# Optimization experiments

Hardware: AMD Instinct MI355X
Metric: run time of the kernel (lower is better)

## Reference

```python
import jax, jax.numpy as jnp
import numpy as np

N_NODES = 100000
N_EDGES = 1600000
N_MOVES = 200000
D = 256          # in_channels
H = 512          # hidden_dim

def setup_inputs() -> dict:
    key = jax.random.key(0)
    ks = jax.random.split(key, 6)
    node_embeddings = jax.random.normal(ks[0], (N_NODES, D), dtype=jnp.float32)
    edge_index = jax.random.randint(ks[1], (2, N_EDGES), 0, N_NODES, dtype=jnp.int64)
    move_edge_idxs = jax.random.randint(ks[2], (N_MOVES,), 0, N_EDGES, dtype=jnp.int64)
    # torch Linear weights: [out, in], scaled like kaiming-uniform-ish
    W1 = jax.random.normal(ks[3], (H, 2 * D), dtype=jnp.float32) * (1.0 / np.sqrt(2 * D))
    b1 = jnp.zeros((H,), dtype=jnp.float32)
    W2 = jax.random.normal(ks[4], (H // 2, H), dtype=jnp.float32) * (1.0 / np.sqrt(H))
    b2 = jnp.zeros((H // 2,), dtype=jnp.float32)
    W3 = jax.random.normal(ks[5], (1, H // 2), dtype=jnp.float32) * (1.0 / np.sqrt(H // 2))
    b3 = jnp.zeros((1,), dtype=jnp.float32)
    return {"node_embeddings": node_embeddings, "edge_index": edge_index,
            "move_edge_idxs": move_edge_idxs, "W1": W1, "b1": b1,
            "W2": W2, "b2": b2, "W3": W3, "b3": b3}

def reference(node_embeddings, edge_index, move_edge_idxs, W1, b1, W2, b2, W3, b3):
    # candidate_moves = edge_index[:, move_edge_idxs].T -> [n_moves, 2]
    src = edge_index[0, move_edge_idxs]          # [n_moves]
    tgt = edge_index[1, move_edge_idxs]          # [n_moves]
    emb_src = node_embeddings[src]               # [n_moves, D]
    emb_tgt = node_embeddings[tgt]               # [n_moves, D]
    x = jnp.concatenate([emb_src, emb_tgt], axis=-1)   # [n_moves, 2D]
    # 3-layer MLP (dropout is identity in eval mode)
    h = jax.nn.relu(x @ W1.T + b1)               # [n_moves, H]
    h = jax.nn.relu(h @ W2.T + b2)               # [n_moves, H//2]
    logits = (h @ W3.T + b3).squeeze(-1)         # [n_moves]
    return logits
```

## Files before the change

kernel.cpp:

```cpp
#include <hip/hip_runtime.h>
#include <hip/hip_bf16.h>

typedef __attribute__((ext_vector_type(4))) float f32x4;
typedef __attribute__((ext_vector_type(8))) short bfrag;
typedef __attribute__((ext_vector_type(4))) float facc;
typedef __attribute__((ext_vector_type(8))) ushort u16x8;

#define N_MOVES 200000
#define N_EDGES 1600000
#define DEMB 256
#define KD 512
#define H1D 512
#define H2D 256
#define MT 64
#define NTHREADS 512

__device__ __forceinline__ ushort f2b(float f) {
  union { float f; unsigned u; } x; x.f = f;
  unsigned r = (x.u + 0x7fffu + ((x.u >> 16) & 1u)) >> 16;
  return (ushort)r;
}
__device__ __forceinline__ float b2f(ushort h) {
  union { unsigned u; float f; } x; x.u = ((unsigned)h) << 16;
  return x.f;
}

__global__ void convert_w(const float* __restrict__ W1, const float* __restrict__ W2,
                          ushort* __restrict__ Wb) {
  int i = (blockIdx.x * 256 + threadIdx.x) * 4;
  const int n1 = H1D * KD;
  if (i < n1) {
    f32x4 v = *(const f32x4*)(W1 + i);
    ushort4 h = { f2b(v.x), f2b(v.y), f2b(v.z), f2b(v.w) };
    *(ushort4*)(Wb + i) = h;
  } else {
    int j = i - n1;
    f32x4 v = *(const f32x4*)(W2 + j);
    ushort4 h = { f2b(v.x), f2b(v.y), f2b(v.z), f2b(v.w) };
    *(ushort4*)(Wb + n1 + j) = h;
  }
}

__global__ void convert_emb(const float* __restrict__ E, ushort* __restrict__ Eb) {
  int i = (blockIdx.x * 256 + threadIdx.x) * 8;
  f32x4 a = *(const f32x4*)(E + i);
  f32x4 b = *(const f32x4*)(E + i + 4);
  u16x8 h = { f2b(a.x), f2b(a.y), f2b(a.z), f2b(a.w),
              f2b(b.x), f2b(b.y), f2b(b.z), f2b(b.w) };
  *(u16x8*)(Eb + i) = h;
}

template<int EMBBF>
__global__ __launch_bounds__(NTHREADS, 2)
void fused_mlp(const float* __restrict__ emb,
               const ushort* __restrict__ embb,
               const int* __restrict__ edge_index,
               const int* __restrict__ move_idx,
               const ushort* __restrict__ W1b,
               const float* __restrict__ b1,
               const ushort* __restrict__ W2b,
               const float* __restrict__ b2,
               const float* __restrict__ W3,
               const float* __restrict__ b3,
               float* __restrict__ out)
{
  __shared__ ushort bufA[MT][KD];
  __shared__ ushort bufB[MT][KD];
  __shared__ int   s_src[MT], s_tgt[MT];
  __shared__ float sW3[H2D];

  const int tid  = threadIdx.x;
  const int lane = tid & 63;
  const int wave = tid >> 6;
  const int m0   = blockIdx.x * MT;

  if (tid < MT) {
    int e = move_idx[m0 + tid];
    s_src[tid] = edge_index[e];
    s_tgt[tid] = edge_index[N_EDGES + e];
  }
  if (tid < H2D) sW3[tid] = W3[tid];
  __syncthreads();

  const int arow = lane & 15;
  const int akE  = (lane >> 4) << 3;
  const int akB  = (lane >> 4) << 4;
  const int nq   = (lane >> 4) << 2;

  const ushort* wp0 = W1b + (size_t)(((wave << 6) + arow) * KD) + akE;
  const ushort* wp1 = wp0 + 16 * KD;
  const ushort* wp2 = wp0 + 32 * KD;
  const ushort* wp3 = wp0 + 48 * KD;

  bfrag bA[4], bB[4];
  bA[0] = *(const bfrag*)(wp0);      bA[1] = *(const bfrag*)(wp1);
  bA[2] = *(const bfrag*)(wp2);      bA[3] = *(const bfrag*)(wp3);
  bB[0] = *(const bfrag*)(wp0 + 32); bB[1] = *(const bfrag*)(wp1 + 32);
  bB[2] = *(const bfrag*)(wp2 + 32); bB[3] = *(const bfrag*)(wp3 + 32);

  if (EMBBF) {
    #pragma unroll
    for (int it = 0; it < 8; ++it) {
      int row  = (wave << 3) + it;
      int gl   = lane ^ (row & 7);
      int node = (gl < 32) ? s_src[row] : s_tgt[row];
      const ushort* gp = embb + (size_t)node * DEMB + ((size_t)(gl & 31) << 3);
      __builtin_amdgcn_global_load_lds(
          (const __attribute__((address_space(1))) void*)gp,
          (__attribute__((address_space(3))) void*)(&bufA[row][0]),
          16, 0, 0);
    }
  } else {
    for (int u = tid; u < MT * 128; u += NTHREADS) {
      int row = u >> 7;
      int c4  = u & 127;
      const float* sp = (c4 < 64) ? (emb + (size_t)s_src[row] * DEMB + (c4 << 2))
                                  : (emb + (size_t)s_tgt[row] * DEMB + ((c4 - 64) << 2));
      f32x4 v = *(const f32x4*)sp;
      ushort4 h = { f2b(v.x), f2b(v.y), f2b(v.z), f2b(v.w) };
      int bo = (c4 << 3) ^ ((row & 7) << 4);
      *(ushort4*)((char*)(&bufA[row][0]) + bo) = h;
    }
  }
  __syncthreads();

  facc acc[4][4];
  #pragma unroll
  for (int ng = 0; ng < 4; ++ng) {
    f32x4 bv = *(const f32x4*)(b1 + (wave << 6) + (ng << 4) + nq);
    #pragma unroll
    for (int mg = 0; mg < 4; ++mg) acc[mg][ng] = bv;
  }

  bfrag aE[4], aO[4];
  #pragma unroll
  for (int mg = 0; mg < 4; ++mg) {
    int row = (mg << 4) + arow;
    int bo = akB ^ ((row & 7) << 4);
    aE[mg] = *(const bfrag*)((const char*)(&bufA[row][0]) + bo);
  }

  #pragma unroll
  for (int kk2 = 0; kk2 < 8; ++kk2) {
    const int kk = kk2 << 1;
    if (kk + 1 < 16) {
      #pragma unroll
      for (int mg = 0; mg < 4; ++mg) {
        int row = (mg << 4) + arow;
        int bo = (((kk + 1) << 6) + akB) ^ ((row & 7) << 4);
        aO[mg] = *(const bfrag*)((const char*)(&bufA[row][0]) + bo);
      }
    }
    __builtin_amdgcn_s_setprio(1);
    #pragma unroll
    for (int mg = 0; mg < 4; ++mg)
      #pragma unroll
      for (int ng = 0; ng < 4; ++ng)
        acc[mg][ng] = __builtin_amdgcn_mfma_f32_16x16x32_bf16(bA[ng], aE[mg], acc[mg][ng], 0, 0, 0);
    __builtin_amdgcn_s_setprio(0);
    if (kk + 2 < 16) {
      bA[0] = *(const bfrag*)(wp0 + ((kk + 2) << 5));
      bA[1] = *(const bfrag*)(wp1 + ((kk + 2) << 5));
      bA[2] = *(const bfrag*)(wp2 + ((kk + 2) << 5));
      bA[3] = *(const bfrag*)(wp3 + ((kk + 2) << 5));
      #pragma unroll
      for (int mg = 0; mg < 4; ++mg) {
        int row = (mg << 4) + arow;
        int bo = (((kk + 2) << 6) + akB) ^ ((row & 7) << 4);
        aE[mg] = *(const bfrag*)((const char*)(&bufA[row][0]) + bo);
      }
    }
    __builtin_amdgcn_s_setprio(1);
    #pragma unroll
    for (int mg = 0; mg < 4; ++mg)
      #pragma unroll
      for (int ng = 0; ng < 4; ++ng)
        acc[mg][ng] = __builtin_amdgcn_mfma_f32_16x16x32_bf16(bB[ng], aO[mg], acc[mg][ng], 0, 0, 0);
    __builtin_amdgcn_s_setprio(0);
    if (kk + 3 < 16) {
      bB[0] = *(const bfrag*)(wp0 + ((kk + 3) << 5));
      bB[1] = *(const bfrag*)(wp1 + ((kk + 3) << 5));
      bB[2] = *(const bfrag*)(wp2 + ((kk + 3) << 5));
      bB[3] = *(const bfrag*)(wp3 + ((kk + 3) << 5));
    }
  }

  const ushort* cp0 = W2b + (size_t)(((wave << 5) + arow) * KD) + akE;
  const ushort* cp1 = cp0 + 16 * KD;
  bfrag cA[2], cB[2];
  cA[0] = *(const bfrag*)(cp0);      cA[1] = *(const bfrag*)(cp1);
  cB[0] = *(const bfrag*)(cp0 + 32); cB[1] = *(const bfrag*)(cp1 + 32);

  #pragma unroll
  for (int mg = 0; mg < 4; ++mg) {
    int m = (mg << 4) + arow;
    #pragma unroll
    for (int ng = 0; ng < 4; ++ng) {
      int nb = (wave << 6) + (ng << 4) + nq;
      ushort4 h;
      h.x = f2b(fmaxf(acc[mg][ng][0], 0.f));
      h.y = f2b(fmaxf(acc[mg][ng][1], 0.f));
      h.z = f2b(fmaxf(acc[mg][ng][2], 0.f));
      h.w = f2b(fmaxf(acc[mg][ng][3], 0.f));
      int bo = (nb << 1) ^ ((m & 7) << 4);
      *(ushort4*)((char*)(&bufB[0][0]) + m * (KD * 2) + bo) = h;
    }
  }
  __syncthreads();

  facc acc2[4][2];
  #pragma unroll
  for (int ng = 0; ng < 2; ++ng) {
    f32x4 bv = *(const f32x4*)(b2 + (wave << 5) + (ng << 4) + nq);
    #pragma unroll
    for (int mg = 0; mg < 4; ++mg) acc2[mg][ng] = bv;
  }

  #pragma unroll
  for (int mg = 0; mg < 4; ++mg) {
    int row = (mg << 4) + arow;
    int bo = akB ^ ((row & 7) << 4);
    aE[mg] = *(const bfrag*)((const char*)(&bufB[row][0]) + bo);
  }

  #pragma unroll
  for (int kk2 = 0; kk2 < 8; ++kk2) {
    const int kk = kk2 << 1;
    if (kk + 1 < 16) {
      #pragma unroll
      for (int mg = 0; mg < 4; ++mg) {
        int row = (mg << 4) + arow;
        int bo = (((kk + 1) << 6) + akB) ^ ((row & 7) << 4);
        aO[mg] = *(const bfrag*)((const char*)(&bufB[row][0]) + bo);
      }
    }
    __builtin_amdgcn_s_setprio(1);
    #pragma unroll
    for (int mg = 0; mg < 4; ++mg)
      #pragma unroll
      for (int ng = 0; ng < 2; ++ng)
        acc2[mg][ng] = __builtin_amdgcn_mfma_f32_16x16x32_bf16(cA[ng], aE[mg], acc2[mg][ng], 0, 0, 0);
    __builtin_amdgcn_s_setprio(0);
    if (kk + 2 < 16) {
      cA[0] = *(const bfrag*)(cp0 + ((kk + 2) << 5));
      cA[1] = *(const bfrag*)(cp1 + ((kk + 2) << 5));
      #pragma unroll
      for (int mg = 0; mg < 4; ++mg) {
        int row = (mg << 4) + arow;
        int bo = (((kk + 2) << 6) + akB) ^ ((row & 7) << 4);
        aE[mg] = *(const bfrag*)((const char*)(&bufB[row][0]) + bo);
      }
    }
    __builtin_amdgcn_s_setprio(1);
    #pragma unroll
    for (int mg = 0; mg < 4; ++mg)
      #pragma unroll
      for (int ng = 0; ng < 2; ++ng)
        acc2[mg][ng] = __builtin_amdgcn_mfma_f32_16x16x32_bf16(cB[ng], aO[mg], acc2[mg][ng], 0, 0, 0);
    __builtin_amdgcn_s_setprio(0);
    if (kk + 3 < 16) {
      cB[0] = *(const bfrag*)(cp0 + ((kk + 3) << 5));
      cB[1] = *(const bfrag*)(cp1 + ((kk + 3) << 5));
    }
  }

  ushort (*H2s)[H2D] = (ushort(*)[H2D])bufA;
  #pragma unroll
  for (int mg = 0; mg < 4; ++mg) {
    int m = (mg << 4) + arow;
    #pragma unroll
    for (int ng = 0; ng < 2; ++ng) {
      int nb = (wave << 5) + (ng << 4) + nq;
      ushort4 h;
      h.x = f2b(fmaxf(acc2[mg][ng][0], 0.f));
      h.y = f2b(fmaxf(acc2[mg][ng][1], 0.f));
      h.z = f2b(fmaxf(acc2[mg][ng][2], 0.f));
      h.w = f2b(fmaxf(acc2[mg][ng][3], 0.f));
      int bo = (nb << 1) ^ ((m & 7) << 4);
      *(ushort4*)((char*)(&H2s[0][0]) + m * (H2D * 2) + bo) = h;
    }
  }
  __syncthreads();

  {
    const float b3v = b3[0];
    int row = tid >> 3;
    int oct = tid & 7;
    float sum = 0.f;
    #pragma unroll
    for (int j = 0; j < 4; ++j) {
      int kb = (oct << 6) + (j << 4);
      int bo = kb ^ ((row & 7) << 4);
      bfrag hv = *(const bfrag*)((const char*)(&H2s[row][0]) + bo);
      int k0 = (oct << 5) + (j << 3);
      #pragma unroll
      for (int e = 0; e < 8; ++e)
        sum += b2f((ushort)hv[e]) * sW3[k0 + e];
    }
    sum += __shfl_xor(sum, 1);
    sum += __shfl_xor(sum, 2);
    sum += __shfl_xor(sum, 4);
    if (oct == 0) out[m0 + row] = sum + b3v;
  }
}

extern "C" void kernel_launch(void* const* d_in, const int* in_sizes, int n_in,
                              void* d_out, int out_size, void* d_ws, size_t ws_size,
                              hipStream_t stream) {
  const float* emb        = (const float*)d_in[0];
  const int*   edge_index = (const int*)d_in[1];
  const int*   move_idx   = (const int*)d_in[2];
  const float* W1         = (const float*)d_in[3];
  const float* b1         = (const float*)d_in[4];
  const float* W2         = (const float*)d_in[5];
  const float* b2         = (const float*)d_in[6];
  const float* W3         = (const float*)d_in[7];
  const float* b3         = (const float*)d_in[8];
  float* out = (float*)d_out;

  ushort* Wb   = (ushort*)d_ws;
  ushort* Embb = Wb + (H1D * KD + H2D * KD);
  const size_t need = (size_t)(H1D * KD + H2D * KD + 100000 * DEMB) * 2;

  convert_w<<<384, 256, 0, stream>>>(W1, W2, Wb);

  if (ws_size >= need) {
    convert_emb<<<12500, 256, 0, stream>>>(emb, Embb);
    fused_mlp<1><<<N_MOVES / MT, NTHREADS, 0, stream>>>(
        emb, Embb, edge_index, move_idx,
        Wb, b1, Wb + H1D * KD, b2, W3, b3, out);
  } else {
    fused_mlp<0><<<N_MOVES / MT, NTHREADS, 0, stream>>>(
        emb, Embb, edge_index, move_idx,
        Wb, b1, Wb + H1D * KD, b2, W3, b3, out);
  }
}
```

Baseline: 524.7 us.

## Double move tile to 128 rows and reuse one LDS buffer for hidden activations

The fused MLP block now handles 128 moves with 1024 threads. Each wave owns a narrower slice of output columns across more rows, so each weight fragment read from global memory is reused over twice as many rows. The separate layer-2 input buffer is dropped, and layer-1 outputs are written back into the gather buffer after an extra barrier, which keeps LDS at one 128KB buffer per block. In exchange, each LDS A-fragment now feeds fewer MFMAs, so there is more LDS traffic per MFMA. A CU likely holds only one large block, so barriers stall all of its waves together. Bounds checks for a partial last tile are added.

```diff
diff --git a/kernel.cpp b/kernel.cpp
--- a/kernel.cpp
+++ b/kernel.cpp
@@ -12,8 +12,8 @@
 #define KD 512
 #define H1D 512
 #define H2D 256
-#define MT 64
-#define NTHREADS 512
+#define MT 128
+#define NTHREADS 1024
 
 __device__ __forceinline__ ushort f2b(float f) {
   union { float f; unsigned u; } x; x.f = f;
@@ -51,7 +51,7 @@
 }
 
 template<int EMBBF>
-__global__ __launch_bounds__(NTHREADS, 2)
+__global__ __launch_bounds__(NTHREADS, 4)
 void fused_mlp(const float* __restrict__ emb,
                const ushort* __restrict__ embb,
                const int* __restrict__ edge_index,
@@ -65,7 +65,6 @@
                float* __restrict__ out)
 {
   __shared__ ushort bufA[MT][KD];
-  __shared__ ushort bufB[MT][KD];
   __shared__ int   s_src[MT], s_tgt[MT];
   __shared__ float sW3[H2D];
 
@@ -75,7 +74,9 @@
   const int m0   = blockIdx.x * MT;
 
   if (tid < MT) {
-    int e = move_idx[m0 + tid];
+    int mi = m0 + tid;
+    if (mi >= N_MOVES) mi = N_MOVES - 1;
+    int e = move_idx[mi];
     s_src[tid] = edge_index[e];
     s_tgt[tid] = edge_index[N_EDGES + e];
   }
@@ -87,16 +88,15 @@
   const int akB  = (lane >> 4) << 4;
   const int nq   = (lane >> 4) << 2;
 
-  const ushort* wp0 = W1b + (size_t)(((wave << 6) + arow) * KD) + akE;
+  const ushort* wp0 = W1b + (size_t)(((wave << 5) + arow) * KD) + akE;
   const ushort* wp1 = wp0 + 16 * KD;
-  const ushort* wp2 = wp0 + 32 * KD;
-  const ushort* wp3 = wp0 + 48 * KD;
-
-  bfrag bA[4], bB[4];
+
+  bfrag bA[2], bB[2];
   bA[0] = *(const bfrag*)(wp0);      bA[1] = *(const bfrag*)(wp1);
-  bA[2] = *(const bfrag*)(wp2);      bA[3] = *(const bfrag*)(wp3);
   bB[0] = *(const bfrag*)(wp0 + 32); bB[1] = *(const bfrag*)(wp1 + 32);
-  bB[2] = *(const bfrag*)(wp2 + 32); bB[3] = *(const bfrag*)(wp3 + 32);
+  f32x4 bv1[2];
+  bv1[0] = *(const f32x4*)(b1 + (wave << 5) + nq);
+  bv1[1] = *(const f32x4*)(b1 + (wave << 5) + 16 + nq);
 
   if (EMBBF) {
     #pragma unroll
@@ -124,17 +124,13 @@
   }
   __syncthreads();
 
-  facc acc[4][4];
-  #pragma unroll
-  for (int ng = 0; ng < 4; ++ng) {
-    f32x4 bv = *(const f32x4*)(b1 + (wave << 6) + (ng << 4) + nq);
-    #pragma unroll
-    for (int mg = 0; mg < 4; ++mg) acc[mg][ng] = bv;
-  }
-
-  bfrag aE[4], aO[4];
-  #pragma unroll
-  for (int mg = 0; mg < 4; ++mg) {
+  facc acc[8][2];
+  #pragma unroll
+  for (int mg = 0; mg < 8; ++mg) { acc[mg][0] = bv1[0]; acc[mg][1] = bv1[1]; }
+
+  bfrag aE[8];
+  #pragma unroll
+  for (int mg = 0; mg < 8; ++mg) {
     int row = (mg << 4) + arow;
     int bo = akB ^ ((row & 7) << 4);
     aE[mg] = *(const bfrag*)((const char*)(&bufA[row][0]) + bo);
@@ -143,142 +139,123 @@
   #pragma unroll
   for (int kk2 = 0; kk2 < 8; ++kk2) {
     const int kk = kk2 << 1;
-    if (kk + 1 < 16) {
-      #pragma unroll
-      for (int mg = 0; mg < 4; ++mg) {
-        int row = (mg << 4) + arow;
-        int bo = (((kk + 1) << 6) + akB) ^ ((row & 7) << 4);
-        aO[mg] = *(const bfrag*)((const char*)(&bufA[row][0]) + bo);
-      }
-    }
     __builtin_amdgcn_s_setprio(1);
     #pragma unroll
-    for (int mg = 0; mg < 4; ++mg)
-      #pragma unroll
-      for (int ng = 0; ng < 4; ++ng)
-        acc[mg][ng] = __builtin_amdgcn_mfma_f32_16x16x32_bf16(bA[ng], aE[mg], acc[mg][ng], 0, 0, 0);
+    for (int mg = 0; mg < 8; ++mg) {
+      acc[mg][0] = __builtin_amdgcn_mfma_f32_16x16x32_bf16(bA[0], aE[mg], acc[mg][0], 0, 0, 0);
+      acc[mg][1] = __builtin_amdgcn_mfma_f32_16x16x32_bf16(bA[1], aE[mg], acc[mg][1], 0, 0, 0);
+    }
     __builtin_amdgcn_s_setprio(0);
+    #pragma unroll
+    for (int mg = 0; mg < 8; ++mg) {
+      int row = (mg << 4) + arow;
+      int bo = (((kk + 1) << 6) + akB) ^ ((row & 7) << 4);
+      aE[mg] = *(const bfrag*)((const char*)(&bufA[row][0]) + bo);
+    }
     if (kk + 2 < 16) {
       bA[0] = *(const bfrag*)(wp0 + ((kk + 2) << 5));
       bA[1] = *(const bfrag*)(wp1 + ((kk + 2) << 5));
-      bA[2] = *(const bfrag*)(wp2 + ((kk + 2) << 5));
-      bA[3] = *(const bfrag*)(wp3 + ((kk + 2) << 5));
+    }
+    __builtin_amdgcn_s_setprio(1);
+    #pragma unroll
+    for (int mg = 0; mg < 8; ++mg) {
+      acc[mg][0] = __builtin_amdgcn_mfma_f32_16x16x32_bf16(bB[0], aE[mg], acc[mg][0], 0, 0, 0);
+      acc[mg][1] = __builtin_amdgcn_mfma_f32_16x16x32_bf16(bB[1], aE[mg], acc[mg][1], 0, 0, 0);
+    }
+    __builtin_amdgcn_s_setprio(0);
+    if (kk2 < 7) {
       #pragma unroll
-      for (int mg = 0; mg < 4; ++mg) {
+      for (int mg = 0; mg < 8; ++mg) {
         int row = (mg << 4) + arow;
         int bo = (((kk + 2) << 6) + akB) ^ ((row & 7) << 4);
         aE[mg] = *(const bfrag*)((const char*)(&bufA[row][0]) + bo);
       }
-    }
-    __builtin_amdgcn_s_setprio(1);
-    #pragma unroll
-    for (int mg = 0; mg < 4; ++mg)
-      #pragma unroll
-      for (int ng = 0; ng < 4; ++ng)
-        acc[mg][ng] = __builtin_amdgcn_mfma_f32_16x16x32_bf16(bB[ng], aO[mg], acc[mg][ng], 0, 0, 0);
-    __builtin_amdgcn_s_setprio(0);
-    if (kk + 3 < 16) {
-      bB[0] = *(const bfrag*)(wp0 + ((kk + 3) << 5));
-      bB[1] = *(const bfrag*)(wp1 + ((kk + 3) << 5));
-      bB[2] = *(const bfrag*)(wp2 + ((kk + 3) << 5));
-      bB[3] = *(const bfrag*)(wp3 + ((kk + 3) << 5));
-    }
-  }
-
-  const ushort* cp0 = W2b + (size_t)(((wave << 5) + arow) * KD) + akE;
-  const ushort* cp1 = cp0 + 16 * KD;
-  bfrag cA[2], cB[2];
-  cA[0] = *(const bfrag*)(cp0);      cA[1] = *(const bfrag*)(cp1);
-  cB[0] = *(const bfrag*)(cp0 + 32); cB[1] = *(const bfrag*)(cp1 + 32);
-
-  #pragma unroll
-  for (int mg = 0; mg < 4; ++mg) {
+      if (kk + 3 < 16) {
+        bB[0] = *(const bfrag*)(wp0 + ((kk + 3) << 5));
+        bB[1] = *(const bfrag*)(wp1 + ((kk + 3) << 5));
+      }
+    }
+  }
+
+  const ushort* cp0 = W2b + (size_t)(((wave << 4) + arow) * KD) + akE;
+  bfrag cA = *(const bfrag*)(cp0);
+  bfrag cB = *(const bfrag*)(cp0 + 32);
+  f32x4 bv2 = *(const f32x4*)(b2 + (wave << 4) + nq);
+
+  __syncthreads();
+
+  #pragma unroll
+  for (int mg = 0; mg < 8; ++mg) {
     int m = (mg << 4) + arow;
     #pragma unroll
-    for (int ng = 0; ng < 4; ++ng) {
-      int nb = (wave << 6) + (ng << 4) + nq;
+    for (int ng = 0; ng < 2; ++ng) {
+      int nb = (wave << 5) + (ng << 4) + nq;
       ushort4 h;
       h.x = f2b(fmaxf(acc[mg][ng][0], 0.f));
       h.y = f2b(fmaxf(acc[mg][ng][1], 0.f));
       h.z = f2b(fmaxf(acc[mg][ng][2], 0.f));
       h.w = f2b(fmaxf(acc[mg][ng][3], 0.f));
       int bo = (nb << 1) ^ ((m & 7) << 4);
-      *(ushort4*)((char*)(&bufB[0][0]) + m * (KD * 2) + bo) = h;
-    }
-  }
-  __syncthreads();
-
-  facc acc2[4][2];
-  #pragma unroll
-  for (int ng = 0; ng < 2; ++ng) {
-    f32x4 bv = *(const f32x4*)(b2 + (wave << 5) + (ng << 4) + nq);
-    #pragma unroll
-    for (int mg = 0; mg < 4; ++mg) acc2[mg][ng] = bv;
-  }
-
-  #pragma unroll
-  for (int mg = 0; mg < 4; ++mg) {
+      *(ushort4*)((char*)(&bufA[0][0]) + m * (KD * 2) + bo) = h;
+    }
+  }
+  __syncthreads();
+
+  facc acc2[8];
+  #pragma unroll
+  for (int mg = 0; mg < 8; ++mg) acc2[mg] = bv2;
+
+  #pragma unroll
+  for (int mg = 0; mg < 8; ++mg) {
     int row = (mg << 4) + arow;
     int bo = akB ^ ((row & 7) << 4);
-    aE[mg] = *(const bfrag*)((const char*)(&bufB[row][0]) + bo);
+    aE[mg] = *(const bfrag*)((const char*)(&bufA[row][0]) + bo);
   }
 
   #pragma unroll
   for (int kk2 = 0; kk2 < 8; ++kk2) {
     const int kk = kk2 << 1;
-    if (kk + 1 < 16) {
+    __builtin_amdgcn_s_setprio(1);
+    #pragma unroll
+    for (int mg = 0; mg < 8; ++mg)
+      acc2[mg] = __builtin_amdgcn_mfma_f32_16x16x32_bf16(cA, aE[mg], acc2[mg], 0, 0, 0);
+    __builtin_amdgcn_s_setprio(0);
+    #pragma unroll
+    for (int mg = 0; mg < 8; ++mg) {
+      int row = (mg << 4) + arow;
+      int bo = (((kk + 1) << 6) + akB) ^ ((row & 7) << 4);
+      aE[mg] = *(const bfrag*)((const char*)(&bufA[row][0]) + bo);
+    }
+    if (kk + 2 < 16) cA = *(const bfrag*)(cp0 + ((kk + 2) << 5));
+    __builtin_amdgcn_s_setprio(1);
+    #pragma unroll
+    for (int mg = 0; mg < 8; ++mg)
+      acc2[mg] = __builtin_amdgcn_mfma_f32_16x16x32_bf16(cB, aE[mg], acc2[mg], 0, 0, 0);
+    __builtin_amdgcn_s_setprio(0);
+    if (kk2 < 7) {
       #pragma unroll
-      for (int mg = 0; mg < 4; ++mg) {
-        int row = (mg << 4) + arow;
-        int bo = (((kk + 1) << 6) + akB) ^ ((row & 7) << 4);
-        aO[mg] = *(const bfrag*)((const char*)(&bufB[row][0]) + bo);
-      }
-    }
-    __builtin_amdgcn_s_setprio(1);
-    #pragma unroll
-    for (int mg = 0; mg < 4; ++mg)
-      #pragma unroll
-      for (int ng = 0; ng < 2; ++ng)
-        acc2[mg][ng] = __builtin_amdgcn_mfma_f32_16x16x32_bf16(cA[ng], aE[mg], acc2[mg][ng], 0, 0, 0);
-    __builtin_amdgcn_s_setprio(0);
-    if (kk + 2 < 16) {
-      cA[0] = *(const bfrag*)(cp0 + ((kk + 2) << 5));
-      cA[1] = *(const bfrag*)(cp1 + ((kk + 2) << 5));
-      #pragma unroll
-      for (int mg = 0; mg < 4; ++mg) {
+      for (int mg = 0; mg < 8; ++mg) {
         int row = (mg << 4) + arow;
         int bo = (((kk + 2) << 6) + akB) ^ ((row & 7) << 4);
-        aE[mg] = *(const bfrag*)((const char*)(&bufB[row][0]) + bo);
+        aE[mg] = *(const bfrag*)((const char*)(&bufA[row][0]) + bo);
       }
-    }
-    __builtin_amdgcn_s_setprio(1);
-    #pragma unroll
-    for (int mg = 0; mg < 4; ++mg)
-      #pragma unroll
-      for (int ng = 0; ng < 2; ++ng)
-        acc2[mg][ng] = __builtin_amdgcn_mfma_f32_16x16x32_bf16(cB[ng], aO[mg], acc2[mg][ng], 0, 0, 0);
-    __builtin_amdgcn_s_setprio(0);
-    if (kk + 3 < 16) {
-      cB[0] = *(const bfrag*)(cp0 + ((kk + 3) << 5));
-      cB[1] = *(const bfrag*)(cp1 + ((kk + 3) << 5));
-    }
-  }
+      if (kk + 3 < 16) cB = *(const bfrag*)(cp0 + ((kk + 3) << 5));
+    }
+  }
+  __syncthreads();
 
   ushort (*H2s)[H2D] = (ushort(*)[H2D])bufA;
   #pragma unroll
-  for (int mg = 0; mg < 4; ++mg) {
+  for (int mg = 0; mg < 8; ++mg) {
     int m = (mg << 4) + arow;
-    #pragma unroll
-    for (int ng = 0; ng < 2; ++ng) {
-      int nb = (wave << 5) + (ng << 4) + nq;
-      ushort4 h;
-      h.x = f2b(fmaxf(acc2[mg][ng][0], 0.f));
-      h.y = f2b(fmaxf(acc2[mg][ng][1], 0.f));
-      h.z = f2b(fmaxf(acc2[mg][ng][2], 0.f));
-      h.w = f2b(fmaxf(acc2[mg][ng][3], 0.f));
-      int bo = (nb << 1) ^ ((m & 7) << 4);
-      *(ushort4*)((char*)(&H2s[0][0]) + m * (H2D * 2) + bo) = h;
-    }
+    int nb = (wave << 4) + nq;
+    ushort4 h;
+    h.x = f2b(fmaxf(acc2[mg][0], 0.f));
+    h.y = f2b(fmaxf(acc2[mg][1], 0.f));
+    h.z = f2b(fmaxf(acc2[mg][2], 0.f));
+    h.w = f2b(fmaxf(acc2[mg][3], 0.f));
+    int bo = (nb << 1) ^ ((m & 7) << 4);
+    *(ushort4*)((char*)(&H2s[0][0]) + m * (H2D * 2) + bo) = h;
   }
   __syncthreads();
 
@@ -300,7 +277,7 @@
     sum += __shfl_xor(sum, 1);
     sum += __shfl_xor(sum, 2);
     sum += __shfl_xor(sum, 4);
-    if (oct == 0) out[m0 + row] = sum + b3v;
+    if (oct == 0 && (m0 + row) < N_MOVES) out[m0 + row] = sum + b3v;
   }
 }
 
@@ -321,16 +298,17 @@
   ushort* Wb   = (ushort*)d_ws;
   ushort* Embb = Wb + (H1D * KD + H2D * KD);
   const size_t need = (size_t)(H1D * KD + H2D * KD + 100000 * DEMB) * 2;
+  const int grid = (N_MOVES + MT - 1) / MT;
 
   convert_w<<<384, 256, 0, stream>>>(W1, W2, Wb);
 
   if (ws_size >= need) {
     convert_emb<<<12500, 256, 0, stream>>>(emb, Embb);
-    fused_mlp<1><<<N_MOVES / MT, NTHREADS, 0, stream>>>(
+    fused_mlp<1><<<grid, NTHREADS, 0, stream>>>(
         emb, Embb, edge_index, move_idx,
         Wb, b1, Wb + H1D * KD, b2, W3, b3, out);
   } else {
-    fused_mlp<0><<<N_MOVES / MT, NTHREADS, 0, stream>>>(
+    fused_mlp<0><<<grid, NTHREADS, 0, stream>>>(
         emb, Embb, edge_index, move_idx,
         Wb, b1, Wb + H1D * KD, b2, W3, b3, out);
   }
```

After: 467.1 us. 11.0% less time.
